# Optimization experiments

Measured on AMD Instinct MI355X. Metric: run time of the kernel, lower is better.

The kernel has to match this reference:

```python
import jax, jax.numpy as jnp
import numpy as np

D_MODEL = 1024
N_HEADS = 16
D_K = D_MODEL // N_HEADS  # 64
D_V = D_MODEL // N_HEADS  # 64
B, S = 2, 2048


def setup_inputs() -> dict:
    key = jax.random.key(0)
    ks = jax.random.split(key, 8)
    inp = {
        "Q": jax.random.normal(ks[0], (B, S, D_MODEL), dtype=jnp.float32),
        "K": jax.random.normal(ks[1], (B, S, D_MODEL), dtype=jnp.float32),
        "V": jax.random.normal(ks[2], (B, S, D_MODEL), dtype=jnp.float32),
        "prev": jax.random.normal(ks[3], (B, N_HEADS, S, S), dtype=jnp.float32) * 0.1,
        # torch nn.Linear weights are [out_features, in_features]
        "W_Q": jax.random.normal(ks[4], (N_HEADS * D_K, D_MODEL), dtype=jnp.float32) / np.sqrt(D_MODEL),
        "W_K": jax.random.normal(ks[5], (N_HEADS * D_K, D_MODEL), dtype=jnp.float32) / np.sqrt(D_MODEL),
        "W_V": jax.random.normal(ks[6], (N_HEADS * D_V, D_MODEL), dtype=jnp.float32) / np.sqrt(D_MODEL),
        "W_O": jax.random.normal(ks[7], (D_MODEL, N_HEADS * D_V), dtype=jnp.float32) / np.sqrt(N_HEADS * D_V),
    }
    return inp


def reference(Q, K, V, prev, W_Q, W_K, W_V, W_O):
    scale = D_K ** (-0.5)
    # projections: x @ W.T, then split heads -> (b, h, s, d)
    q = jnp.einsum('bsm,em->bse', Q, W_Q).reshape(B, S, N_HEADS, D_K).transpose(0, 2, 1, 3)
    k = jnp.einsum('bsm,em->bse', K, W_K).reshape(B, S, N_HEADS, D_K).transpose(0, 2, 1, 3)
    v = jnp.einsum('bsm,em->bse', V, W_V).reshape(B, S, N_HEADS, D_V).transpose(0, 2, 1, 3)
    scores = jnp.einsum('bhqd,bhkd->bhqk', q, k) * scale + prev
    attn = jax.nn.softmax(scores, axis=-1)  # attn_dropout = 0 (eval)
    context = jnp.einsum('bhqk,bhkd->bhqd', attn, v)
    context = context.transpose(0, 2, 1, 3).reshape(B, S, N_HEADS * D_V)
    output = jnp.einsum('bse,me->bsm', context, W_O)  # proj_dropout = 0 (eval)
    return (output, attn, scores)
```

## Files before the change

### kernel.cpp

```cpp
#include <hip/hip_runtime.h>

#define S_LEN 2048
#define NH 16
#define DH 64
#define DM 1024
#define NB 2
#define BS 4096

typedef __attribute__((ext_vector_type(4))) float f32x4;
typedef __attribute__((ext_vector_type(8))) short bfrag;

__device__ __forceinline__ unsigned short f2bf(float f) {
    unsigned u = __builtin_bit_cast(unsigned, f);
    u += 0x7FFFu + ((u >> 16) & 1u);
    return (unsigned short)(u >> 16);
}

__device__ __forceinline__ void bar_lgkm() {
    asm volatile("s_waitcnt lgkmcnt(0)" ::: "memory");
    __builtin_amdgcn_s_barrier();
}

__global__ __launch_bounds__(256) void gemm_qkv(const float* __restrict__ Qi,
                                                const float* __restrict__ Ki,
                                                const float* __restrict__ Vi,
                                                const float* __restrict__ Wq,
                                                const float* __restrict__ Wk,
                                                const float* __restrict__ Wv,
                                                unsigned short* __restrict__ qh,
                                                unsigned short* __restrict__ kh,
                                                unsigned short* __restrict__ vT) {
    const int z = blockIdx.z;
    const float* A = (z == 0) ? Qi : (z == 1) ? Ki : Vi;
    const float* B = (z == 0) ? Wq : (z == 1) ? Wk : Wv;
    const int tid = threadIdx.x, lane = tid & 63;
    const int l15 = lane & 15, lhi = lane >> 4;
    const int w = tid >> 6, wr = w >> 1, wc = w & 1;
    const int m0 = blockIdx.y * 128, n0 = blockIdx.x * 64;
    const int K = DM;

    __shared__ unsigned short sA[2][128 * 64];
    __shared__ unsigned short sB[2][64 * 64];

    float4 va[8], vb[4];
#pragma unroll
    for (int i = 0; i < 8; ++i) {
        int c = i * 256 + tid, row = c >> 4, col4 = c & 15;
        va[i] = *reinterpret_cast<const float4*>(A + (size_t)(m0 + row) * K + col4 * 4);
    }
#pragma unroll
    for (int i = 0; i < 4; ++i) {
        int c = i * 256 + tid, row = c >> 4, col4 = c & 15;
        vb[i] = *reinterpret_cast<const float4*>(B + (size_t)(n0 + row) * K + col4 * 4);
    }

    f32x4 acc[4][2];
#pragma unroll
    for (int i = 0; i < 4; ++i)
#pragma unroll
        for (int j = 0; j < 2; ++j) acc[i][j] = (f32x4){0.f, 0.f, 0.f, 0.f};

    for (int t = 0; t < 16; ++t) {
        unsigned short* pA = sA[t & 1];
        unsigned short* pB = sB[t & 1];
#pragma unroll
        for (int i = 0; i < 8; ++i) {
            int c = i * 256 + tid, row = c >> 4, col4 = c & 15;
            ushort4 o;
            o.x = f2bf(va[i].x); o.y = f2bf(va[i].y); o.z = f2bf(va[i].z); o.w = f2bf(va[i].w);
            *reinterpret_cast<ushort4*>(pA + row * 64 + ((col4 * 4) ^ ((row & 7) * 8))) = o;
        }
#pragma unroll
        for (int i = 0; i < 4; ++i) {
            int c = i * 256 + tid, row = c >> 4, col4 = c & 15;
            ushort4 o;
            o.x = f2bf(vb[i].x); o.y = f2bf(vb[i].y); o.z = f2bf(vb[i].z); o.w = f2bf(vb[i].w);
            *reinterpret_cast<ushort4*>(pB + row * 64 + ((col4 * 4) ^ ((row & 7) * 8))) = o;
        }
        if (t < 15) {
            const int k0 = (t + 1) * 64;
#pragma unroll
            for (int i = 0; i < 8; ++i) {
                int c = i * 256 + tid, row = c >> 4, col4 = c & 15;
                va[i] = *reinterpret_cast<const float4*>(A + (size_t)(m0 + row) * K + k0 + col4 * 4);
            }
#pragma unroll
            for (int i = 0; i < 4; ++i) {
                int c = i * 256 + tid, row = c >> 4, col4 = c & 15;
                vb[i] = *reinterpret_cast<const float4*>(B + (size_t)(n0 + row) * K + k0 + col4 * 4);
            }
        }
        bar_lgkm();
#pragma unroll
        for (int kk = 0; kk < 2; ++kk) {
            bfrag a[4], b[2];
#pragma unroll
            for (int f = 0; f < 4; ++f) {
                int ra = wr * 64 + f * 16 + l15;
                a[f] = *reinterpret_cast<const bfrag*>(pA + ra * 64 +
                                                       ((kk * 32 + lhi * 8) ^ ((ra & 7) * 8)));
            }
#pragma unroll
            for (int f = 0; f < 2; ++f) {
                int rb = wc * 32 + f * 16 + l15;
                b[f] = *reinterpret_cast<const bfrag*>(pB + rb * 64 +
                                                       ((kk * 32 + lhi * 8) ^ ((rb & 7) * 8)));
            }
#pragma unroll
            for (int fm = 0; fm < 4; ++fm)
#pragma unroll
                for (int fn = 0; fn < 2; ++fn)
                    acc[fm][fn] =
                        __builtin_amdgcn_mfma_f32_16x16x32_bf16(a[fm], b[fn], acc[fm][fn], 0, 0, 0);
        }
    }

    if (z == 2) {
#pragma unroll
        for (int fm = 0; fm < 4; ++fm)
#pragma unroll
            for (int fn = 0; fn < 2; ++fn) {
                int sbase = m0 + wr * 64 + fm * 16 + (lhi << 2);
                int gcol = n0 + wc * 32 + fn * 16 + l15;
                int b = sbase >> 11, s = sbase & 2047, h = gcol >> 6, d = gcol & 63;
                ushort4 o;
                o.x = f2bf(acc[fm][fn][0]); o.y = f2bf(acc[fm][fn][1]);
                o.z = f2bf(acc[fm][fn][2]); o.w = f2bf(acc[fm][fn][3]);
                *reinterpret_cast<ushort4*>(vT + ((size_t)(b * NH + h) * DH + d) * S_LEN + s) = o;
            }
    } else {
        unsigned short* Out = (z == 0) ? qh : kh;
#pragma unroll
        for (int fm = 0; fm < 4; ++fm)
#pragma unroll
            for (int fn = 0; fn < 2; ++fn)
#pragma unroll
                for (int r = 0; r < 4; ++r) {
                    int grow = m0 + wr * 64 + fm * 16 + (lhi << 2) + r;
                    int gcol = n0 + wc * 32 + fn * 16 + l15;
                    int b = grow >> 11, s = grow & 2047, h = gcol >> 6, d = gcol & 63;
                    Out[((size_t)(b * NH + h) * S_LEN + s) * DH + d] = f2bf(acc[fm][fn][r]);
                }
    }
}

__global__ __launch_bounds__(256) void gemm_out(const unsigned short* __restrict__ A,
                                                const float* __restrict__ B,
                                                float* __restrict__ Out) {
    const int tid = threadIdx.x, lane = tid & 63;
    const int l15 = lane & 15, lhi = lane >> 4;
    const int w = tid >> 6, wr = w >> 1, wc = w & 1;
    const int m0 = blockIdx.y * 128, n0 = blockIdx.x * 64;
    const int K = DM, N = DM;

    __shared__ unsigned short sA[2][128 * 64];
    __shared__ unsigned short sB[2][64 * 64];

    int4 va[4];
    float4 vb[4];
#pragma unroll
    for (int i = 0; i < 4; ++i) {
        int c = i * 256 + tid, row = c >> 3, col8 = c & 7;
        va[i] = *reinterpret_cast<const int4*>(A + (size_t)(m0 + row) * K + col8 * 8);
    }
#pragma unroll
    for (int i = 0; i < 4; ++i) {
        int c = i * 256 + tid, row = c >> 4, col4 = c & 15;
        vb[i] = *reinterpret_cast<const float4*>(B + (size_t)(n0 + row) * K + col4 * 4);
    }

    f32x4 acc[4][2];
#pragma unroll
    for (int i = 0; i < 4; ++i)
#pragma unroll
        for (int j = 0; j < 2; ++j) acc[i][j] = (f32x4){0.f, 0.f, 0.f, 0.f};

    for (int t = 0; t < 16; ++t) {
        unsigned short* pA = sA[t & 1];
        unsigned short* pB = sB[t & 1];
#pragma unroll
        for (int i = 0; i < 4; ++i) {
            int c = i * 256 + tid, row = c >> 3, col8 = c & 7;
            *reinterpret_cast<int4*>(pA + row * 64 + ((col8 * 8) ^ ((row & 7) * 8))) = va[i];
        }
#pragma unroll
        for (int i = 0; i < 4; ++i) {
            int c = i * 256 + tid, row = c >> 4, col4 = c & 15;
            ushort4 o;
            o.x = f2bf(vb[i].x); o.y = f2bf(vb[i].y); o.z = f2bf(vb[i].z); o.w = f2bf(vb[i].w);
            *reinterpret_cast<ushort4*>(pB + row * 64 + ((col4 * 4) ^ ((row & 7) * 8))) = o;
        }
        if (t < 15) {
            const int k0 = (t + 1) * 64;
#pragma unroll
            for (int i = 0; i < 4; ++i) {
                int c = i * 256 + tid, row = c >> 3, col8 = c & 7;
                va[i] = *reinterpret_cast<const int4*>(A + (size_t)(m0 + row) * K + k0 + col8 * 8);
            }
#pragma unroll
            for (int i = 0; i < 4; ++i) {
                int c = i * 256 + tid, row = c >> 4, col4 = c & 15;
                vb[i] = *reinterpret_cast<const float4*>(B + (size_t)(n0 + row) * K + k0 + col4 * 4);
            }
        }
        bar_lgkm();
#pragma unroll
        for (int kk = 0; kk < 2; ++kk) {
            bfrag a[4], b[2];
#pragma unroll
            for (int f = 0; f < 4; ++f) {
                int ra = wr * 64 + f * 16 + l15;
                a[f] = *reinterpret_cast<const bfrag*>(pA + ra * 64 +
                                                       ((kk * 32 + lhi * 8) ^ ((ra & 7) * 8)));
            }
#pragma unroll
            for (int f = 0; f < 2; ++f) {
                int rb = wc * 32 + f * 16 + l15;
                b[f] = *reinterpret_cast<const bfrag*>(pB + rb * 64 +
                                                       ((kk * 32 + lhi * 8) ^ ((rb & 7) * 8)));
            }
#pragma unroll
            for (int fm = 0; fm < 4; ++fm)
#pragma unroll
                for (int fn = 0; fn < 2; ++fn)
                    acc[fm][fn] =
                        __builtin_amdgcn_mfma_f32_16x16x32_bf16(a[fm], b[fn], acc[fm][fn], 0, 0, 0);
        }
    }

#pragma unroll
    for (int fm = 0; fm < 4; ++fm)
#pragma unroll
        for (int fn = 0; fn < 2; ++fn)
#pragma unroll
            for (int r = 0; r < 4; ++r) {
                int grow = m0 + wr * 64 + fm * 16 + (lhi << 2) + r;
                int gcol = n0 + wc * 32 + fn * 16 + l15;
                Out[(size_t)grow * N + gcol] = acc[fm][fn][r];
            }
}

__global__ __launch_bounds__(256, 4) void attn_fused(const unsigned short* __restrict__ qh,
                                                     const unsigned short* __restrict__ kh,
                                                     const unsigned short* __restrict__ vT,
                                                     const float* __restrict__ prev,
                                                     float* __restrict__ scores,
                                                     float* __restrict__ attn,
                                                     unsigned short* __restrict__ ctx) {
    const int z = blockIdx.z;
    const int m0 = blockIdx.x * 64;
    const int tid = threadIdx.x;
    const int lane = tid & 63;
    const int w = tid >> 6;
    const int l15 = lane & 15, lhi = lane >> 4;

    __shared__ unsigned short smem[16384];
    unsigned short* sQ = smem;
    unsigned short* sK = smem + 4096;
    unsigned short* sV = smem;
    unsigned short* sP = smem + 8192;

    const unsigned short* Qz = qh + (size_t)z * S_LEN * DH;
    const unsigned short* Kz = kh + (size_t)z * S_LEN * DH;
    const unsigned short* Vz = vT + (size_t)z * DH * S_LEN;
    const size_t zbase = (size_t)z * S_LEN * S_LEN;
    const float scale = 0.125f;
    const int rowb = w * 16 + lhi * 4;

#pragma unroll
    for (int i = 0; i < 2; ++i) {
        int c = i * 256 + tid, row = c >> 3, col8 = c & 7;
        *reinterpret_cast<int4*>(sQ + row * 64 + ((col8 * 8) ^ ((row & 7) * 8))) =
            *reinterpret_cast<const int4*>(Qz + (size_t)(m0 + row) * DH + col8 * 8);
    }

    float m_r[4], l_r[4];
#pragma unroll
    for (int r = 0; r < 4; ++r) { m_r[r] = -1e30f; l_r[r] = 0.f; }

    int4 kreg[4];
#pragma unroll
    for (int i = 0; i < 4; ++i) {
        int c = i * 256 + tid, row = c >> 3, col8 = c & 7;
        kreg[i] = *reinterpret_cast<const int4*>(Kz + (size_t)row * DH + col8 * 8);
    }
    float pv[32];
#pragma unroll
    for (int fn = 0; fn < 8; ++fn)
#pragma unroll
        for (int r = 0; r < 4; ++r)
            pv[fn * 4 + r] = __builtin_nontemporal_load(
                prev + zbase + (size_t)(m0 + rowb + r) * S_LEN + fn * 16 + l15);

    for (int kt = 0; kt < S_LEN / 128; ++kt) {
        const int n0 = kt * 128;
        bar_lgkm();
#pragma unroll
        for (int i = 0; i < 4; ++i) {
            int c = i * 256 + tid, row = c >> 3, col8 = c & 7;
            *reinterpret_cast<int4*>(sK + row * 64 + ((col8 * 8) ^ ((row & 7) * 8))) = kreg[i];
        }
        if (kt < 15) {
            const int n1 = n0 + 128;
#pragma unroll
            for (int i = 0; i < 4; ++i) {
                int c = i * 256 + tid, row = c >> 3, col8 = c & 7;
                kreg[i] = *reinterpret_cast<const int4*>(Kz + (size_t)(n1 + row) * DH + col8 * 8);
            }
        }
        bar_lgkm();

        f32x4 acc[8];
#pragma unroll
        for (int fn = 0; fn < 8; ++fn) acc[fn] = (f32x4){0.f, 0.f, 0.f, 0.f};
#pragma unroll
        for (int kk = 0; kk < 2; ++kk) {
            int ra = w * 16 + l15;
            bfrag a = *reinterpret_cast<const bfrag*>(sQ + ra * 64 +
                                                      ((kk * 32 + lhi * 8) ^ ((ra & 7) * 8)));
            bfrag b[8];
#pragma unroll
            for (int f = 0; f < 8; ++f) {
                int rb = f * 16 + l15;
                b[f] = *reinterpret_cast<const bfrag*>(sK + rb * 64 +
                                                       ((kk * 32 + lhi * 8) ^ ((rb & 7) * 8)));
            }
#pragma unroll
            for (int fn = 0; fn < 8; ++fn)
                acc[fn] = __builtin_amdgcn_mfma_f32_16x16x32_bf16(a, b[fn], acc[fn], 0, 0, 0);
        }

#pragma unroll
        for (int fn = 0; fn < 8; ++fn)
#pragma unroll
            for (int r = 0; r < 4; ++r) acc[fn][r] = acc[fn][r] * scale + pv[fn * 4 + r];
        if (kt < 15) {
            const int n1 = n0 + 128;
#pragma unroll
            for (int fn = 0; fn < 8; ++fn)
#pragma unroll
                for (int r = 0; r < 4; ++r)
                    pv[fn * 4 + r] = __builtin_nontemporal_load(
                        prev + zbase + (size_t)(m0 + rowb + r) * S_LEN + n1 + fn * 16 + l15);
        }
#pragma unroll
        for (int fn = 0; fn < 8; ++fn)
#pragma unroll
            for (int r = 0; r < 4; ++r)
                scores[zbase + (size_t)(m0 + rowb + r) * S_LEN + n0 + fn * 16 + l15] = acc[fn][r];
#pragma unroll
        for (int r = 0; r < 4; ++r) {
            float pm = acc[0][r];
#pragma unroll
            for (int fn = 1; fn < 8; ++fn) pm = fmaxf(pm, acc[fn][r]);
            pm = fmaxf(pm, __shfl_xor(pm, 1));
            pm = fmaxf(pm, __shfl_xor(pm, 2));
            pm = fmaxf(pm, __shfl_xor(pm, 4));
            pm = fmaxf(pm, __shfl_xor(pm, 8));
            float mnew = fmaxf(m_r[r], pm);
            float psum = 0.f;
#pragma unroll
            for (int fn = 0; fn < 8; ++fn) psum += __expf(acc[fn][r] - mnew);
            psum += __shfl_xor(psum, 1);
            psum += __shfl_xor(psum, 2);
            psum += __shfl_xor(psum, 4);
            psum += __shfl_xor(psum, 8);
            l_r[r] = l_r[r] * __expf(m_r[r] - mnew) + psum;
            m_r[r] = mnew;
        }
    }

    float inv_l[4];
#pragma unroll
    for (int r = 0; r < 4; ++r) inv_l[r] = 1.0f / l_r[r];

    f32x4 acco[4];
#pragma unroll
    for (int fn = 0; fn < 4; ++fn) acco[fn] = (f32x4){0.f, 0.f, 0.f, 0.f};

    int4 vreg[4];
#pragma unroll
    for (int i = 0; i < 4; ++i) {
        int c = i * 256 + tid, row = c >> 4, col8 = c & 15;
        vreg[i] = *reinterpret_cast<const int4*>(Vz + (size_t)row * S_LEN + col8 * 8);
    }
    float sv[32];
#pragma unroll
    for (int fn = 0; fn < 8; ++fn)
#pragma unroll
        for (int r = 0; r < 4; ++r)
            sv[fn * 4 + r] = scores[zbase + (size_t)(m0 + rowb + r) * S_LEN + fn * 16 + l15];

    for (int kt = 0; kt < S_LEN / 128; ++kt) {
        const int n0 = kt * 128;
        bar_lgkm();
#pragma unroll
        for (int i = 0; i < 4; ++i) {
            int c = i * 256 + tid, row = c >> 4, col8 = c & 15;
            *reinterpret_cast<int4*>(sV + row * 128 + ((col8 ^ (row & 7)) << 3)) = vreg[i];
        }
        if (kt < 15) {
            const int n1 = n0 + 128;
#pragma unroll
            for (int i = 0; i < 4; ++i) {
                int c = i * 256 + tid, row = c >> 4, col8 = c & 15;
                vreg[i] = *reinterpret_cast<const int4*>(Vz + (size_t)row * S_LEN + n1 + col8 * 8);
            }
        }
#pragma unroll
        for (int fn = 0; fn < 8; ++fn)
#pragma unroll
            for (int r = 0; r < 4; ++r) {
                float p = __expf(sv[fn * 4 + r] - m_r[r]) * inv_l[r];
                __builtin_nontemporal_store(
                    p, attn + zbase + (size_t)(m0 + rowb + r) * S_LEN + n0 + fn * 16 + l15);
                int prow = rowb + r, pcol = fn * 16 + l15;
                sP[prow * 128 + (((pcol >> 3) ^ (prow & 7)) << 3) + (pcol & 7)] = f2bf(p);
            }
        if (kt < 15) {
            const int n1 = n0 + 128;
#pragma unroll
            for (int fn = 0; fn < 8; ++fn)
#pragma unroll
                for (int r = 0; r < 4; ++r)
                    sv[fn * 4 + r] =
                        scores[zbase + (size_t)(m0 + rowb + r) * S_LEN + n1 + fn * 16 + l15];
        }
        bar_lgkm();
#pragma unroll
        for (int kk = 0; kk < 4; ++kk) {
            int ra = w * 16 + l15;
            bfrag a = *reinterpret_cast<const bfrag*>(sP + ra * 128 +
                                                      (((kk * 4 + lhi) ^ (ra & 7)) << 3));
            bfrag b[4];
#pragma unroll
            for (int f = 0; f < 4; ++f) {
                int rb = f * 16 + l15;
                b[f] = *reinterpret_cast<const bfrag*>(sV + rb * 128 +
                                                       (((kk * 4 + lhi) ^ (rb & 7)) << 3));
            }
#pragma unroll
            for (int fn = 0; fn < 4; ++fn)
                acco[fn] = __builtin_amdgcn_mfma_f32_16x16x32_bf16(a, b[fn], acco[fn], 0, 0, 0);
        }
    }

    const int b = z >> 4, h = z & 15;
#pragma unroll
    for (int fn = 0; fn < 4; ++fn)
#pragma unroll
        for (int r = 0; r < 4; ++r) {
            int s = m0 + rowb + r;
            int d = fn * 16 + l15;
            ctx[((size_t)(b * S_LEN + s)) * DM + h * DH + d] = f2bf(acco[fn][r]);
        }
}

extern "C" void kernel_launch(void* const* d_in, const int* in_sizes, int n_in, void* d_out,
                              int out_size, void* d_ws, size_t ws_size, hipStream_t stream) {
    const float* Q = (const float*)d_in[0];
    const float* K = (const float*)d_in[1];
    const float* V = (const float*)d_in[2];
    const float* prev = (const float*)d_in[3];
    const float* Wq = (const float*)d_in[4];
    const float* Wk = (const float*)d_in[5];
    const float* Wv = (const float*)d_in[6];
    const float* Wo = (const float*)d_in[7];

    float* out = (float*)d_out;
    float* attn = out + (size_t)BS * DM;
    float* scores = attn + (size_t)NB * NH * S_LEN * S_LEN;

    unsigned short* ws = (unsigned short*)d_ws;
    unsigned short* qh = ws;
    unsigned short* kh = qh + (size_t)BS * DM;
    unsigned short* vT = kh + (size_t)BS * DM;
    unsigned short* ctx = vT + (size_t)BS * DM;

    dim3 gq(DM / 64, BS / 128, 3);
    gemm_qkv<<<gq, 256, 0, stream>>>(Q, K, V, Wq, Wk, Wv, qh, kh, vT);

    dim3 ga(S_LEN / 64, 1, NB * NH);
    attn_fused<<<ga, 256, 0, stream>>>(qh, kh, vT, prev, scores, attn, ctx);

    dim3 gp(DM / 64, BS / 128, 1);
    gemm_out<<<gp, 256, 0, stream>>>(ctx, Wo, out);
}
```

Measured before the change: 755.5 us.

## Pre-cast GEMM inputs to bf16 and use direct global-to-LDS loads with 128x128 tiles

Adds separate cast kernels that convert the Q/K/V activations and all weight matrices to bf16 in the workspace before the projection GEMMs. The GEMMs then stage tiles with global_load_lds directly into swizzled LDS and grow the tile from 128x64 to 128x128. The aim is to drop the per-tile fp32-to-bf16 conversion and register staging inside the GEMM loop and to improve operand reuse. In exchange it adds seven extra launches and an extra pass over the inputs, and it removes double buffering in favour of two barriers per k-step.

```diff
diff --git a/kernel.cpp b/kernel.cpp
--- a/kernel.cpp
+++ b/kernel.cpp
@@ -21,107 +21,90 @@
     __builtin_amdgcn_s_barrier();
 }
 
-__global__ __launch_bounds__(256) void gemm_qkv(const float* __restrict__ Qi,
-                                                const float* __restrict__ Ki,
-                                                const float* __restrict__ Vi,
-                                                const float* __restrict__ Wq,
-                                                const float* __restrict__ Wk,
-                                                const float* __restrict__ Wv,
+__device__ __forceinline__ void gld16(const unsigned short* g, unsigned short* l) {
+    __builtin_amdgcn_global_load_lds((const __attribute__((address_space(1))) void*)g,
+                                     (__attribute__((address_space(3))) void*)l, 16, 0, 0);
+}
+
+__global__ __launch_bounds__(256) void cast_kernel(const float* __restrict__ in,
+                                                   unsigned short* __restrict__ out, int n4) {
+    int i = blockIdx.x * 256 + threadIdx.x;
+    if (i < n4) {
+        float4 v = reinterpret_cast<const float4*>(in)[i];
+        ushort4 o;
+        o.x = f2bf(v.x); o.y = f2bf(v.y); o.z = f2bf(v.z); o.w = f2bf(v.w);
+        reinterpret_cast<ushort4*>(out)[i] = o;
+    }
+}
+
+__global__ __launch_bounds__(256) void gemm_qkv(const unsigned short* __restrict__ Qc,
+                                                const unsigned short* __restrict__ Kc,
+                                                const unsigned short* __restrict__ Vc,
+                                                const unsigned short* __restrict__ Wqc,
+                                                const unsigned short* __restrict__ Wkc,
+                                                const unsigned short* __restrict__ Wvc,
                                                 unsigned short* __restrict__ qh,
                                                 unsigned short* __restrict__ kh,
                                                 unsigned short* __restrict__ vT) {
     const int z = blockIdx.z;
-    const float* A = (z == 0) ? Qi : (z == 1) ? Ki : Vi;
-    const float* B = (z == 0) ? Wq : (z == 1) ? Wk : Wv;
+    const unsigned short* A = (z == 0) ? Qc : (z == 1) ? Kc : Vc;
+    const unsigned short* B = (z == 0) ? Wqc : (z == 1) ? Wkc : Wvc;
     const int tid = threadIdx.x, lane = tid & 63;
     const int l15 = lane & 15, lhi = lane >> 4;
     const int w = tid >> 6, wr = w >> 1, wc = w & 1;
-    const int m0 = blockIdx.y * 128, n0 = blockIdx.x * 64;
+    const int m0 = blockIdx.y * 128, n0 = blockIdx.x * 128;
     const int K = DM;
-
-    __shared__ unsigned short sA[2][128 * 64];
-    __shared__ unsigned short sB[2][64 * 64];
-
-    float4 va[8], vb[4];
-#pragma unroll
-    for (int i = 0; i < 8; ++i) {
-        int c = i * 256 + tid, row = c >> 4, col4 = c & 15;
-        va[i] = *reinterpret_cast<const float4*>(A + (size_t)(m0 + row) * K + col4 * 4);
-    }
-#pragma unroll
-    for (int i = 0; i < 4; ++i) {
-        int c = i * 256 + tid, row = c >> 4, col4 = c & 15;
-        vb[i] = *reinterpret_cast<const float4*>(B + (size_t)(n0 + row) * K + col4 * 4);
-    }
-
-    f32x4 acc[4][2];
+    const int lr8 = lane >> 3;
+    const int csw = (lane & 7) ^ lr8;
+
+    __shared__ unsigned short sA[128 * 64];
+    __shared__ unsigned short sB[128 * 64];
+
+    f32x4 acc[4][4];
 #pragma unroll
     for (int i = 0; i < 4; ++i)
 #pragma unroll
-        for (int j = 0; j < 2; ++j) acc[i][j] = (f32x4){0.f, 0.f, 0.f, 0.f};
+        for (int j = 0; j < 4; ++j) acc[i][j] = (f32x4){0.f, 0.f, 0.f, 0.f};
 
     for (int t = 0; t < 16; ++t) {
-        unsigned short* pA = sA[t & 1];
-        unsigned short* pB = sB[t & 1];
-#pragma unroll
-        for (int i = 0; i < 8; ++i) {
-            int c = i * 256 + tid, row = c >> 4, col4 = c & 15;
-            ushort4 o;
-            o.x = f2bf(va[i].x); o.y = f2bf(va[i].y); o.z = f2bf(va[i].z); o.w = f2bf(va[i].w);
-            *reinterpret_cast<ushort4*>(pA + row * 64 + ((col4 * 4) ^ ((row & 7) * 8))) = o;
-        }
+        const int k0 = t * 64;
 #pragma unroll
         for (int i = 0; i < 4; ++i) {
-            int c = i * 256 + tid, row = c >> 4, col4 = c & 15;
-            ushort4 o;
-            o.x = f2bf(vb[i].x); o.y = f2bf(vb[i].y); o.z = f2bf(vb[i].z); o.w = f2bf(vb[i].w);
-            *reinterpret_cast<ushort4*>(pB + row * 64 + ((col4 * 4) ^ ((row & 7) * 8))) = o;
-        }
-        if (t < 15) {
-            const int k0 = (t + 1) * 64;
-#pragma unroll
-            for (int i = 0; i < 8; ++i) {
-                int c = i * 256 + tid, row = c >> 4, col4 = c & 15;
-                va[i] = *reinterpret_cast<const float4*>(A + (size_t)(m0 + row) * K + k0 + col4 * 4);
-            }
-#pragma unroll
-            for (int i = 0; i < 4; ++i) {
-                int c = i * 256 + tid, row = c >> 4, col4 = c & 15;
-                vb[i] = *reinterpret_cast<const float4*>(B + (size_t)(n0 + row) * K + k0 + col4 * 4);
-            }
-        }
-        bar_lgkm();
+            int g = w * 4 + i;
+            int row = g * 8 + lr8;
+            gld16(A + (size_t)(m0 + row) * K + k0 + csw * 8, sA + g * 512);
+            gld16(B + (size_t)(n0 + row) * K + k0 + csw * 8, sB + g * 512);
+        }
+        __syncthreads();
 #pragma unroll
         for (int kk = 0; kk < 2; ++kk) {
-            bfrag a[4], b[2];
+            bfrag a[4], b[4];
 #pragma unroll
             for (int f = 0; f < 4; ++f) {
                 int ra = wr * 64 + f * 16 + l15;
-                a[f] = *reinterpret_cast<const bfrag*>(pA + ra * 64 +
-                                                       ((kk * 32 + lhi * 8) ^ ((ra & 7) * 8)));
-            }
-#pragma unroll
-            for (int f = 0; f < 2; ++f) {
-                int rb = wc * 32 + f * 16 + l15;
-                b[f] = *reinterpret_cast<const bfrag*>(pB + rb * 64 +
-                                                       ((kk * 32 + lhi * 8) ^ ((rb & 7) * 8)));
+                a[f] = *reinterpret_cast<const bfrag*>(
+                    sA + ra * 64 + (((kk * 4 + lhi) ^ (ra & 7)) << 3));
+                int rb = wc * 64 + f * 16 + l15;
+                b[f] = *reinterpret_cast<const bfrag*>(
+                    sB + rb * 64 + (((kk * 4 + lhi) ^ (rb & 7)) << 3));
             }
 #pragma unroll
             for (int fm = 0; fm < 4; ++fm)
 #pragma unroll
-                for (int fn = 0; fn < 2; ++fn)
+                for (int fn = 0; fn < 4; ++fn)
                     acc[fm][fn] =
                         __builtin_amdgcn_mfma_f32_16x16x32_bf16(a[fm], b[fn], acc[fm][fn], 0, 0, 0);
         }
+        __syncthreads();
     }
 
     if (z == 2) {
 #pragma unroll
         for (int fm = 0; fm < 4; ++fm)
 #pragma unroll
-            for (int fn = 0; fn < 2; ++fn) {
+            for (int fn = 0; fn < 4; ++fn) {
                 int sbase = m0 + wr * 64 + fm * 16 + (lhi << 2);
-                int gcol = n0 + wc * 32 + fn * 16 + l15;
+                int gcol = n0 + wc * 64 + fn * 16 + l15;
                 int b = sbase >> 11, s = sbase & 2047, h = gcol >> 6, d = gcol & 63;
                 ushort4 o;
                 o.x = f2bf(acc[fm][fn][0]); o.y = f2bf(acc[fm][fn][1]);
@@ -133,11 +116,11 @@
 #pragma unroll
         for (int fm = 0; fm < 4; ++fm)
 #pragma unroll
-            for (int fn = 0; fn < 2; ++fn)
+            for (int fn = 0; fn < 4; ++fn)
 #pragma unroll
                 for (int r = 0; r < 4; ++r) {
                     int grow = m0 + wr * 64 + fm * 16 + (lhi << 2) + r;
-                    int gcol = n0 + wc * 32 + fn * 16 + l15;
+                    int gcol = n0 + wc * 64 + fn * 16 + l15;
                     int b = grow >> 11, s = grow & 2047, h = gcol >> 6, d = gcol & 63;
                     Out[((size_t)(b * NH + h) * S_LEN + s) * DH + d] = f2bf(acc[fm][fn][r]);
                 }
@@ -145,97 +128,65 @@
 }
 
 __global__ __launch_bounds__(256) void gemm_out(const unsigned short* __restrict__ A,
-                                                const float* __restrict__ B,
+                                                const unsigned short* __restrict__ B,
                                                 float* __restrict__ Out) {
     const int tid = threadIdx.x, lane = tid & 63;
     const int l15 = lane & 15, lhi = lane >> 4;
     const int w = tid >> 6, wr = w >> 1, wc = w & 1;
-    const int m0 = blockIdx.y * 128, n0 = blockIdx.x * 64;
+    const int m0 = blockIdx.y * 128, n0 = blockIdx.x * 128;
     const int K = DM, N = DM;
-
-    __shared__ unsigned short sA[2][128 * 64];
-    __shared__ unsigned short sB[2][64 * 64];
-
-    int4 va[4];
-    float4 vb[4];
-#pragma unroll
-    for (int i = 0; i < 4; ++i) {
-        int c = i * 256 + tid, row = c >> 3, col8 = c & 7;
-        va[i] = *reinterpret_cast<const int4*>(A + (size_t)(m0 + row) * K + col8 * 8);
-    }
-#pragma unroll
-    for (int i = 0; i < 4; ++i) {
-        int c = i * 256 + tid, row = c >> 4, col4 = c & 15;
-        vb[i] = *reinterpret_cast<const float4*>(B + (size_t)(n0 + row) * K + col4 * 4);
-    }
-
-    f32x4 acc[4][2];
+    const int lr8 = lane >> 3;
+    const int csw = (lane & 7) ^ lr8;
+
+    __shared__ unsigned short sA[128 * 64];
+    __shared__ unsigned short sB[128 * 64];
+
+    f32x4 acc[4][4];
 #pragma unroll
     for (int i = 0; i < 4; ++i)
 #pragma unroll
-        for (int j = 0; j < 2; ++j) acc[i][j] = (f32x4){0.f, 0.f, 0.f, 0.f};
+        for (int j = 0; j < 4; ++j) acc[i][j] = (f32x4){0.f, 0.f, 0.f, 0.f};
 
     for (int t = 0; t < 16; ++t) {
-        unsigned short* pA = sA[t & 1];
-        unsigned short* pB = sB[t & 1];
+        const int k0 = t * 64;
 #pragma unroll
         for (int i = 0; i < 4; ++i) {
-            int c = i * 256 + tid, row = c >> 3, col8 = c & 7;
-            *reinterpret_cast<int4*>(pA + row * 64 + ((col8 * 8) ^ ((row & 7) * 8))) = va[i];
-        }
-#pragma unroll
-        for (int i = 0; i < 4; ++i) {
-            int c = i * 256 + tid, row = c >> 4, col4 = c & 15;
-            ushort4 o;
-            o.x = f2bf(vb[i].x); o.y = f2bf(vb[i].y); o.z = f2bf(vb[i].z); o.w = f2bf(vb[i].w);
-            *reinterpret_cast<ushort4*>(pB + row * 64 + ((col4 * 4) ^ ((row & 7) * 8))) = o;
-        }
-        if (t < 15) {
-            const int k0 = (t + 1) * 64;
-#pragma unroll
-            for (int i = 0; i < 4; ++i) {
-                int c = i * 256 + tid, row = c >> 3, col8 = c & 7;
-                va[i] = *reinterpret_cast<const int4*>(A + (size_t)(m0 + row) * K + k0 + col8 * 8);
-            }
-#pragma unroll
-            for (int i = 0; i < 4; ++i) {
-                int c = i * 256 + tid, row = c >> 4, col4 = c & 15;
-                vb[i] = *reinterpret_cast<const float4*>(B + (size_t)(n0 + row) * K + k0 + col4 * 4);
-            }
-        }
-        bar_lgkm();
+            int g = w * 4 + i;
+            int row = g * 8 + lr8;
+            gld16(A + (size_t)(m0 + row) * K + k0 + csw * 8, sA + g * 512);
+            gld16(B + (size_t)(n0 + row) * K + k0 + csw * 8, sB + g * 512);
+        }
+        __syncthreads();
 #pragma unroll
         for (int kk = 0; kk < 2; ++kk) {
-            bfrag a[4], b[2];
+            bfrag a[4], b[4];
 #pragma unroll
             for (int f = 0; f < 4; ++f) {
                 int ra = wr * 64 + f * 16 + l15;
-                a[f] = *reinterpret_cast<const bfrag*>(pA + ra * 64 +
-                                                       ((kk * 32 + lhi * 8) ^ ((ra & 7) * 8)));
-            }
-#pragma unroll
-            for (int f = 0; f < 2; ++f) {
-                int rb = wc * 32 + f * 16 + l15;
-                b[f] = *reinterpret_cast<const bfrag*>(pB + rb * 64 +
-                                                       ((kk * 32 + lhi * 8) ^ ((rb & 7) * 8)));
+                a[f] = *reinterpret_cast<const bfrag*>(
+                    sA + ra * 64 + (((kk * 4 + lhi) ^ (ra & 7)) << 3));
+                int rb = wc * 64 + f * 16 + l15;
+                b[f] = *reinterpret_cast<const bfrag*>(
+                    sB + rb * 64 + (((kk * 4 + lhi) ^ (rb & 7)) << 3));
             }
 #pragma unroll
             for (int fm = 0; fm < 4; ++fm)
 #pragma unroll
-                for (int fn = 0; fn < 2; ++fn)
+                for (int fn = 0; fn < 4; ++fn)
                     acc[fm][fn] =
                         __builtin_amdgcn_mfma_f32_16x16x32_bf16(a[fm], b[fn], acc[fm][fn], 0, 0, 0);
         }
+        __syncthreads();
     }
 
 #pragma unroll
     for (int fm = 0; fm < 4; ++fm)
 #pragma unroll
-        for (int fn = 0; fn < 2; ++fn)
+        for (int fn = 0; fn < 4; ++fn)
 #pragma unroll
             for (int r = 0; r < 4; ++r) {
                 int grow = m0 + wr * 64 + fm * 16 + (lhi << 2) + r;
-                int gcol = n0 + wc * 32 + fn * 16 + l15;
+                int gcol = n0 + wc * 64 + fn * 16 + l15;
                 Out[(size_t)grow * N + gcol] = acc[fm][fn][r];
             }
 }
@@ -472,17 +423,32 @@
     float* scores = attn + (size_t)NB * NH * S_LEN * S_LEN;
 
     unsigned short* ws = (unsigned short*)d_ws;
-    unsigned short* qh = ws;
+    unsigned short* Qc = ws;
+    unsigned short* Kc = Qc + (size_t)BS * DM;
+    unsigned short* Vc = Kc + (size_t)BS * DM;
+    unsigned short* Wqc = Vc + (size_t)BS * DM;
+    unsigned short* Wkc = Wqc + (size_t)DM * DM;
+    unsigned short* Wvc = Wkc + (size_t)DM * DM;
+    unsigned short* Woc = Wvc + (size_t)DM * DM;
+    unsigned short* qh = Woc + (size_t)DM * DM;
     unsigned short* kh = qh + (size_t)BS * DM;
     unsigned short* vT = kh + (size_t)BS * DM;
     unsigned short* ctx = vT + (size_t)BS * DM;
 
-    dim3 gq(DM / 64, BS / 128, 3);
-    gemm_qkv<<<gq, 256, 0, stream>>>(Q, K, V, Wq, Wk, Wv, qh, kh, vT);
+    cast_kernel<<<BS * DM / 4 / 256, 256, 0, stream>>>(Q, Qc, BS * DM / 4);
+    cast_kernel<<<BS * DM / 4 / 256, 256, 0, stream>>>(K, Kc, BS * DM / 4);
+    cast_kernel<<<BS * DM / 4 / 256, 256, 0, stream>>>(V, Vc, BS * DM / 4);
+    cast_kernel<<<DM * DM / 4 / 256, 256, 0, stream>>>(Wq, Wqc, DM * DM / 4);
+    cast_kernel<<<DM * DM / 4 / 256, 256, 0, stream>>>(Wk, Wkc, DM * DM / 4);
+    cast_kernel<<<DM * DM / 4 / 256, 256, 0, stream>>>(Wv, Wvc, DM * DM / 4);
+    cast_kernel<<<DM * DM / 4 / 256, 256, 0, stream>>>(Wo, Woc, DM * DM / 4);
+
+    dim3 gq(DM / 128, BS / 128, 3);
+    gemm_qkv<<<gq, 256, 0, stream>>>(Qc, Kc, Vc, Wqc, Wkc, Wvc, qh, kh, vT);
 
     dim3 ga(S_LEN / 64, 1, NB * NH);
     attn_fused<<<ga, 256, 0, stream>>>(qh, kh, vT, prev, scores, attn, ctx);
 
-    dim3 gp(DM / 64, BS / 128, 1);
-    gemm_out<<<gp, 256, 0, stream>>>(ctx, Wo, out);
-}
+    dim3 gp(DM / 128, BS / 128, 1);
+    gemm_out<<<gp, 256, 0, stream>>>(ctx, Woc, out);
+}
```

Result: faster. 727.9 us (-3.7%).
